# Performance work log

Measured on AMD Instinct MI355X. Metric: run time of the kernel, lower is better.

## Reference

```python
import jax, jax.numpy as jnp
import numpy as np

N = 8192        # n_nodes
NFEAT = 512
NHID = 256
AVG_DEG = 32
K = 64          # mean_kwargs k
TEMP = 1.0      # mean_kwargs temperature


def setup_inputs() -> dict:
    key = jax.random.key(0)
    ks = jax.random.split(key, 5)
    x = jax.random.normal(ks[0], (N, NFEAT), jnp.float32)
    edge_index = jax.random.randint(ks[1], (2, N * AVG_DEG), 0, N, dtype=jnp.int64)
    W1 = jax.random.normal(ks[2], (NFEAT, NHID), jnp.float32) / np.sqrt(NFEAT)
    b1 = jnp.zeros((NHID,), jnp.float32)
    W2 = jax.random.normal(ks[3], (NHID, NHID), jnp.float32) / np.sqrt(NHID)
    b2 = jnp.zeros((NHID,), jnp.float32)
    return {"x": x, "edge_index": edge_index, "W1": W1, "b1": b1, "W2": W2, "b2": b2}


def _gcn_norm(edge_index, n, dtype):
    # PyG gcn_norm: add self-loops (weight 1), deg over col, sym normalization
    loops = jnp.arange(n, dtype=edge_index.dtype)
    row = jnp.concatenate([edge_index[0], loops])
    col = jnp.concatenate([edge_index[1], loops])
    w = jnp.ones(row.shape[0], dtype)
    deg = jnp.zeros((n,), dtype).at[col].add(w)
    dis = jnp.where(deg > 0, jax.lax.rsqrt(jnp.where(deg > 0, deg, 1.0)), 0.0)
    return row, col, dis[row] * w * dis[col]


def _soft_k_medoid(row, col, w, x):
    # soft_weighted_medoid_k_neighborhood(A, x, k=K, temperature=TEMP, with_weight_correction=True)
    n, d = x.shape
    A = jnp.zeros((n, n), x.dtype).at[row, col].add(w)   # coalesced dense adjacency
    topk_a, topk_idx = jax.lax.top_k(A, K)               # [n, K] neighbor weights / ids
    xk = x[topk_idx]                                     # [n, K, d]
    sq = jnp.sum(xk * xk, axis=-1)                       # [n, K]
    G = jnp.einsum('nkd,nld->nkl', xk, xk)               # Gram per node
    d2 = jnp.maximum(sq[:, :, None] + sq[:, None, :] - 2.0 * G, 0.0)
    pos = d2 > 0
    dist = jnp.where(pos, jnp.sqrt(jnp.where(pos, d2, 1.0)), 0.0)  # safe sqrt (grad-safe)
    # weighted sum of distances to each top-k candidate j: c[n,j] = sum_l a[n,l] * ||x_l - x_j||
    c = jnp.einsum('nl,nlj->nj', topk_a, dist)
    c = jnp.where(topk_a == 0, jnp.finfo(x.dtype).max, c)
    soft = jax.nn.softmax(-c / TEMP, axis=-1)            # [n, K]
    soft = soft * topk_a                                 # with_weight_correction
    soft = soft / jnp.sum(soft, axis=-1, keepdims=True)
    row_sum = jnp.sum(A, axis=-1)                        # preserve neighborhood mass
    return row_sum[:, None] * jnp.einsum('nk,nkd->nd', soft, xk)


def reference(x, edge_index, W1, b1, W2, b2):
    n = x.shape[0]
    row, col, w = _gcn_norm(edge_index, n, x.dtype)
    h = jax.nn.relu(_soft_k_medoid(row, col, w, x @ W1) + b1)   # gc1 + relu (dropout: eval = identity)
    return jax.nn.relu(_soft_k_medoid(row, col, w, h @ W2) + b2)  # gc2 + relu
```

## Files before the change

### kernel.cpp

```cpp
#include <hip/hip_runtime.h>

typedef _Float16 half2v __attribute__((ext_vector_type(2)));
typedef _Float16 half4 __attribute__((ext_vector_type(4)));
typedef _Float16 half8 __attribute__((ext_vector_type(8)));
typedef float f32x4 __attribute__((ext_vector_type(4)));

#define NNODE 8192
#define NHID  256
#define RCAP  128
#define KCAP  64

__global__ void k_init(int* deg, int* rowcnt, int* flag, const void* edges) {
    int i = blockIdx.x * blockDim.x + threadIdx.x;
    if (i < NNODE) { deg[i] = 0; rowcnt[i] = 0; }
    if (i == 0) {
        const long long* e = (const long long*)edges;
        int ok = 1;
        for (int k = 0; k < 64; ++k) { long long v = e[k]; if (v < 0 || v >= NNODE) ok = 0; }
        *flag = ok;
    }
}

__global__ void k_build(const void* edges, const int* flag, int* rowcnt, int* nbr,
                        int* deg, int E) {
    int i = blockIdx.x * blockDim.x + threadIdx.x;
    int total = E + NNODE;
    if (i >= total) return;
    int r, c;
    if (i < E) {
        if (*flag) {
            const long long* e = (const long long*)edges;
            r = (int)e[i]; c = (int)e[E + i];
        } else {
            const int* e = (const int*)edges;
            r = e[i]; c = e[E + i];
        }
    } else { r = i - E; c = r; }
    int pos = atomicAdd(&rowcnt[r], 1);
    if (pos < RCAP) nbr[r * RCAP + pos] = c;
    atomicAdd(&deg[c], 1);
}

__global__ __launch_bounds__(128) void k_dedup(const int* __restrict__ nbr,
                                               const int* __restrict__ rowcnt,
                                               const int* __restrict__ deg,
                                               int* __restrict__ cols,
                                               float* __restrict__ wout,
                                               float* __restrict__ rsum) {
    __shared__ int lc[RCAP];
    __shared__ float lw[RCAP];
    __shared__ unsigned char kp[RCAP];
    __shared__ int s_cw[2];
    __shared__ float s_rw[2];
    const int r = blockIdx.x, t = threadIdx.x;
    const int wid = t >> 6, lane = t & 63;
    int n = rowcnt[r]; if (n > RCAP) n = RCAP;
    if (t < n) lc[t] = nbr[r * RCAP + t];
    __syncthreads();
    float dr = 1.f / sqrtf((float)deg[r]);
    bool keep = false; float wv = 0.f;
    if (t < n) {
        int c = lc[t];
        int mult = 0; bool first = true;
        for (int i = 0; i < n; ++i) {
            int ci = lc[i];
            if (ci == c) { mult++; if (i < t) first = false; }
        }
        keep = first;
        if (first) wv = (float)mult * dr * (1.f / sqrtf((float)deg[c]));
    }
    kp[t] = keep ? 1 : 0; lw[t] = wv;
    float rv = wv;
#pragma unroll
    for (int d = 1; d < 64; d <<= 1) rv += __shfl_xor(rv, d, 64);
    unsigned long long b = __ballot(keep);
    int pre = __popcll(b & ((1ull << lane) - 1ull));
    int cw = __popcll(b);
    if (lane == 0) { s_cw[wid] = cw; s_rw[wid] = rv; }
    __syncthreads();
    int total = s_cw[0] + s_cw[1];
    if (t == 0) rsum[r] = s_rw[0] + s_rw[1];
    const int base = r * KCAP;
    if (total <= KCAP) {
        int off = (wid ? s_cw[0] : 0) + pre;
        if (keep) { cols[base + off] = lc[t]; wout[base + off] = wv; }
        for (int m = total + t; m < KCAP; m += 128) { cols[base + m] = r; wout[base + m] = 0.f; }
    } else if (t == 0) {
        for (int s = 0; s < KCAP; ++s) {
            int best = -1;
            for (int i = 0; i < n; ++i) {
                if (!kp[i]) continue;
                if (best < 0 || lw[i] > lw[best] ||
                    (lw[i] == lw[best] && lc[i] < lc[best])) best = i;
            }
            cols[base + s] = lc[best]; wout[base + s] = lw[best]; kp[best] = 0;
        }
    }
}

__global__ void k_splitT(const float* __restrict__ W, _Float16* __restrict__ hiT, int Kdim) {
    int idx = blockIdx.x * 256 + threadIdx.x;
    if (idx >= Kdim * NHID) return;
    int k = idx >> 8, n = idx & 255;
    hiT[(size_t)n * Kdim + k] = (_Float16)W[idx];
}

#define GLS 72

__global__ __launch_bounds__(256) void k_gemm(
    const float* __restrict__ Af32, const _Float16* __restrict__ Ahi,
    const _Float16* __restrict__ BT, _Float16* __restrict__ Chi, int K, int af32) {
    __shared__ _Float16 sA[64][GLS];
    __shared__ _Float16 sB[64][GLS];
    const int t = threadIdx.x;
    const int bm = blockIdx.x * 64, bn = blockIdx.y * 64;
    const int lane = t & 63, L15 = lane & 15, q = lane >> 4;
    const int w = t >> 6, wr = w >> 1, wc = w & 1;
    f32x4 acc[2][2];
#pragma unroll
    for (int a = 0; a < 2; ++a)
#pragma unroll
        for (int b = 0; b < 2; ++b) acc[a][b] = (f32x4){0.f, 0.f, 0.f, 0.f};

    for (int k0 = 0; k0 < K; k0 += 64) {
        if (af32) {
#pragma unroll
            for (int i = 0; i < 4; ++i) {
                int row = i * 16 + (t >> 4), kc = (t & 15) * 4;
                float4 v = *(const float4*)(Af32 + (size_t)(bm + row) * K + k0 + kc);
                half4 h;
                h[0] = (_Float16)v.x; h[1] = (_Float16)v.y;
                h[2] = (_Float16)v.z; h[3] = (_Float16)v.w;
                *(half4*)&sA[row][kc] = h;
            }
        } else {
#pragma unroll
            for (int i = 0; i < 2; ++i) {
                int row = i * 32 + (t >> 3), ch = t & 7;
                *(half8*)&sA[row][ch * 8] =
                    *(const half8*)(Ahi + (size_t)(bm + row) * K + k0 + ch * 8);
            }
        }
#pragma unroll
        for (int i = 0; i < 2; ++i) {
            int row = i * 32 + (t >> 3), ch = t & 7;
            *(half8*)&sB[row][ch * 8] =
                *(const half8*)(BT + (size_t)(bn + row) * K + k0 + ch * 8);
        }
        __syncthreads();
#pragma unroll
        for (int ks = 0; ks < 2; ++ks) {
            const int ko = ks * 32 + q * 8;
            half8 ah[2], bh[2];
#pragma unroll
            for (int tr = 0; tr < 2; ++tr)
                ah[tr] = *(const half8*)&sA[32 * wr + 16 * tr + L15][ko];
#pragma unroll
            for (int tc = 0; tc < 2; ++tc)
                bh[tc] = *(const half8*)&sB[32 * wc + 16 * tc + L15][ko];
#pragma unroll
            for (int tr = 0; tr < 2; ++tr)
#pragma unroll
                for (int tc = 0; tc < 2; ++tc)
                    acc[tr][tc] = __builtin_amdgcn_mfma_f32_16x16x32_f16(ah[tr], bh[tc], acc[tr][tc], 0, 0, 0);
        }
        __syncthreads();
    }
#pragma unroll
    for (int tr = 0; tr < 2; ++tr)
#pragma unroll
        for (int tc = 0; tc < 2; ++tc)
#pragma unroll
            for (int r = 0; r < 4; ++r) {
                int rowg = bm + 32 * wr + 16 * tr + q * 4 + r;
                int colg = bn + 32 * wc + 16 * tc + L15;
                Chi[(size_t)rowg * NHID + colg] = (_Float16)acc[tr][tc][r];
            }
}

#define MS 264

__global__ __launch_bounds__(256, 4) void k_medoid(
    const _Float16* __restrict__ Xhi,
    const float* __restrict__ bias,
    float* __restrict__ OutF, _Float16* __restrict__ OutHi,
    const int* __restrict__ cols, const float* __restrict__ wts,
    const float* __restrict__ rsum, int writeH) {
    __shared__ _Float16 sh[64][MS];
    __shared__ float s_a[64];
    __shared__ float s_sq[64];
    __shared__ float s_cpart[2][64];
    __shared__ float s_u[64];
    __shared__ int   s_cols[64];
    __shared__ float s_red[4][288];

    const int node = blockIdx.x;
    const int t = threadIdx.x;
    const int w = t >> 6, lane = t & 63;
    const int L15 = lane & 15, q = lane >> 4;
    const int wr = w >> 1, wc = w & 1;

    if (t < 64) { s_cols[t] = cols[node * KCAP + t]; s_a[t] = wts[node * KCAP + t]; }
    __syncthreads();

    {
        const int ch = t & 31, rr = t >> 5;
#pragma unroll
        for (int i = 0; i < 8; ++i) {
            int l = i * 8 + rr;
            *(half8*)&sh[l][ch * 8] = *(const half8*)(Xhi + ((size_t)s_cols[l] << 8) + ch * 8);
        }
    }
    __syncthreads();

    f32x4 acc[2][2];
#pragma unroll
    for (int a = 0; a < 2; ++a)
#pragma unroll
        for (int b = 0; b < 2; ++b) acc[a][b] = (f32x4){0.f, 0.f, 0.f, 0.f};
#pragma unroll
    for (int ks = 0; ks < 8; ++ks) {
        const int ko = ks * 32 + q * 8;
        half8 ah[2], bh[2];
#pragma unroll
        for (int tr = 0; tr < 2; ++tr) ah[tr] = *(const half8*)&sh[32 * wr + 16 * tr + L15][ko];
#pragma unroll
        for (int tc = 0; tc < 2; ++tc) bh[tc] = *(const half8*)&sh[32 * wc + 16 * tc + L15][ko];
#pragma unroll
        for (int tr = 0; tr < 2; ++tr)
#pragma unroll
            for (int tc = 0; tc < 2; ++tc)
                acc[tr][tc] = __builtin_amdgcn_mfma_f32_16x16x32_f16(ah[tr], bh[tc], acc[tr][tc], 0, 0, 0);
    }

#pragma unroll
    for (int tr = 0; tr < 2; ++tr)
#pragma unroll
        for (int tc = 0; tc < 2; ++tc)
            if (32 * wr + 16 * tr == 32 * wc + 16 * tc) {
#pragma unroll
                for (int r = 0; r < 4; ++r)
                    if (L15 == q * 4 + r) s_sq[32 * wr + 16 * tr + L15] = acc[tr][tc][r];
            }
    __syncthreads();

#pragma unroll
    for (int tc = 0; tc < 2; ++tc) {
        const int colg = 32 * wc + 16 * tc + L15;
        const float sqc = s_sq[colg];
        float pj = 0.f;
#pragma unroll
        for (int tr = 0; tr < 2; ++tr)
#pragma unroll
            for (int r = 0; r < 4; ++r) {
                int rowg = 32 * wr + 16 * tr + q * 4 + r;
                float d2 = s_sq[rowg] + sqc - 2.f * acc[tr][tc][r];
                float dist = d2 > 0.f ? __builtin_amdgcn_sqrtf(d2) : 0.f;
                pj = fmaf(s_a[rowg], dist, pj);
            }
        pj += __shfl_xor(pj, 16, 64);
        pj += __shfl_xor(pj, 32, 64);
        if (q == 0) s_cpart[wr][colg] = pj;
    }
    __syncthreads();

    if (w == 0) {
        int j = lane;
        float c = s_cpart[0][j] + s_cpart[1][j];
        float aj = s_a[j];
        bool valid = aj > 0.f;
        float cv = valid ? c : 3.4e38f;
        float mn = cv;
#pragma unroll
        for (int d = 1; d < 64; d <<= 1) mn = fminf(mn, __shfl_xor(mn, d, 64));
        float e = valid ? __expf(mn - c) * aj : 0.f;
        float s = e;
#pragma unroll
        for (int d = 1; d < 64; d <<= 1) s += __shfl_xor(s, d, 64);
        s_u[j] = e * (rsum[node] / s);
    }
    __syncthreads();

    const int oct = t & 31, jb = t >> 5;
    float accd[8] = {0.f, 0.f, 0.f, 0.f, 0.f, 0.f, 0.f, 0.f};
#pragma unroll
    for (int jj = 0; jj < 8; ++jj) {
        int j = jb * 8 + jj;
        float u = s_u[j];
        half8 xv = *(const half8*)&sh[j][8 * oct];
#pragma unroll
        for (int e = 0; e < 8; ++e) accd[e] = fmaf(u, (float)xv[e], accd[e]);
    }
#pragma unroll
    for (int e = 0; e < 8; ++e) accd[e] += __shfl_xor(accd[e], 32, 64);
    if (lane < 32) {
#pragma unroll
        for (int e = 0; e < 8; ++e) s_red[w][9 * oct + e] = accd[e];
    }
    __syncthreads();
    const int idx = 9 * (t >> 3) + (t & 7);
    float o = s_red[0][idx] + s_red[1][idx] + s_red[2][idx] + s_red[3][idx];
    float res = fmaxf(o + bias[t], 0.f);
    size_t oi = (size_t)node * NHID + t;
    if (writeH) OutHi[oi] = (_Float16)res;
    else        OutF[oi] = res;
}

extern "C" void kernel_launch(void* const* d_in, const int* in_sizes, int n_in,
                              void* d_out, int out_size, void* d_ws, size_t ws_size,
                              hipStream_t stream) {
    const float* x  = (const float*)d_in[0];
    const void*  ei = d_in[1];
    const float* W1 = (const float*)d_in[2];
    const float* b1 = (const float*)d_in[3];
    const float* W2 = (const float*)d_in[4];
    const float* b2 = (const float*)d_in[5];
    float* out = (float*)d_out;
    const int E = in_sizes[1] / 2;

    char* p = (char*)d_ws;
    auto alloc = [&](size_t bytes) { char* q = p; p += (bytes + 255) & ~(size_t)255; return q; };
    int*      deg    = (int*)alloc((size_t)NNODE * 4);
    int*      rowcnt = (int*)alloc((size_t)NNODE * 4);
    int*      flag   = (int*)alloc(256);
    int*      colsA  = (int*)alloc((size_t)NNODE * KCAP * 4);
    float*    wA     = (float*)alloc((size_t)NNODE * KCAP * 4);
    float*    rsum   = (float*)alloc((size_t)NNODE * 4);
    _Float16* w1T    = (_Float16*)alloc((size_t)512 * NHID * 2);
    _Float16* w2T    = (_Float16*)alloc((size_t)NHID * NHID * 2);
    _Float16* X1hi   = (_Float16*)alloc((size_t)NNODE * NHID * 2);
    _Float16* Hhi    = (_Float16*)alloc((size_t)NNODE * NHID * 2);
    int* nbr = (int*)alloc((size_t)NNODE * RCAP * 4);

    k_init<<<(NNODE + 255) / 256, 256, 0, stream>>>(deg, rowcnt, flag, ei);
    k_build<<<(E + NNODE + 255) / 256, 256, 0, stream>>>(ei, flag, rowcnt, nbr, deg, E);
    k_dedup<<<NNODE, 128, 0, stream>>>(nbr, rowcnt, deg, colsA, wA, rsum);

    k_splitT<<<(512 * NHID + 255) / 256, 256, 0, stream>>>(W1, w1T, 512);
    k_splitT<<<(NHID * NHID + 255) / 256, 256, 0, stream>>>(W2, w2T, 256);

    k_gemm<<<dim3(NNODE / 64, NHID / 64), 256, 0, stream>>>(x, nullptr, w1T, X1hi, 512, 1);
    k_medoid<<<NNODE, 256, 0, stream>>>(X1hi, b1, nullptr, Hhi, colsA, wA, rsum, 1);
    k_gemm<<<dim3(NNODE / 64, NHID / 64), 256, 0, stream>>>(nullptr, Hhi, w2T, X1hi, 256, 0);
    k_medoid<<<NNODE, 256, 0, stream>>>(X1hi, b2, out, nullptr, colsA, wA, rsum, 0);
}
```

Measured before the change: 218.4 us.

## Merge independent setup kernels, pack dedup rows, compute squared norms at load

Independent setup work is merged into fewer launches: init plus both weight transposes share one kernel, and the edge-list build shares another with the first GEMM through block-index partitioning. The dedup kernel now handles two rows per 256-thread block. The medoid kernel computes squared norms with shuffle reductions while loading neighbor rows, which removes a barrier after the Gram MFMA. The aim is to cut launch overhead and serialization, at the cost of mixed workloads per launch and norms taken from fp16 values rather than from the Gram diagonal.

New measurement: 240.0 us. +9.9%, slower.

```diff
diff --git a/kernel.cpp b/kernel.cpp
--- a/kernel.cpp
+++ b/kernel.cpp
@@ -1,6 +1,5 @@
 #include <hip/hip_runtime.h>
 
-typedef _Float16 half2v __attribute__((ext_vector_type(2)));
 typedef _Float16 half4 __attribute__((ext_vector_type(4)));
 typedef _Float16 half8 __attribute__((ext_vector_type(8)));
 typedef float f32x4 __attribute__((ext_vector_type(4)));
@@ -10,117 +9,47 @@
 #define RCAP  128
 #define KCAP  64
 
-__global__ void k_init(int* deg, int* rowcnt, int* flag, const void* edges) {
-    int i = blockIdx.x * blockDim.x + threadIdx.x;
-    if (i < NNODE) { deg[i] = 0; rowcnt[i] = 0; }
-    if (i == 0) {
-        const long long* e = (const long long*)edges;
-        int ok = 1;
-        for (int k = 0; k < 64; ++k) { long long v = e[k]; if (v < 0 || v >= NNODE) ok = 0; }
-        *flag = ok;
-    }
-}
-
-__global__ void k_build(const void* edges, const int* flag, int* rowcnt, int* nbr,
-                        int* deg, int E) {
-    int i = blockIdx.x * blockDim.x + threadIdx.x;
-    int total = E + NNODE;
-    if (i >= total) return;
-    int r, c;
-    if (i < E) {
-        if (*flag) {
+__global__ __launch_bounds__(256) void k_fused1(
+    int* deg, int* rowcnt, int* flag, const void* edges,
+    const float* __restrict__ W1, _Float16* __restrict__ w1T,
+    const float* __restrict__ W2, _Float16* __restrict__ w2T) {
+    const int b = blockIdx.x, t = threadIdx.x;
+    if (b < 32) {
+        int i = b * 256 + t;
+        deg[i] = 0; rowcnt[i] = 0;
+        if (i == 0) {
             const long long* e = (const long long*)edges;
-            r = (int)e[i]; c = (int)e[E + i];
-        } else {
-            const int* e = (const int*)edges;
-            r = e[i]; c = e[E + i];
-        }
-    } else { r = i - E; c = r; }
-    int pos = atomicAdd(&rowcnt[r], 1);
-    if (pos < RCAP) nbr[r * RCAP + pos] = c;
-    atomicAdd(&deg[c], 1);
-}
-
-__global__ __launch_bounds__(128) void k_dedup(const int* __restrict__ nbr,
-                                               const int* __restrict__ rowcnt,
-                                               const int* __restrict__ deg,
-                                               int* __restrict__ cols,
-                                               float* __restrict__ wout,
-                                               float* __restrict__ rsum) {
-    __shared__ int lc[RCAP];
-    __shared__ float lw[RCAP];
-    __shared__ unsigned char kp[RCAP];
-    __shared__ int s_cw[2];
-    __shared__ float s_rw[2];
-    const int r = blockIdx.x, t = threadIdx.x;
-    const int wid = t >> 6, lane = t & 63;
-    int n = rowcnt[r]; if (n > RCAP) n = RCAP;
-    if (t < n) lc[t] = nbr[r * RCAP + t];
-    __syncthreads();
-    float dr = 1.f / sqrtf((float)deg[r]);
-    bool keep = false; float wv = 0.f;
-    if (t < n) {
-        int c = lc[t];
-        int mult = 0; bool first = true;
-        for (int i = 0; i < n; ++i) {
-            int ci = lc[i];
-            if (ci == c) { mult++; if (i < t) first = false; }
-        }
-        keep = first;
-        if (first) wv = (float)mult * dr * (1.f / sqrtf((float)deg[c]));
-    }
-    kp[t] = keep ? 1 : 0; lw[t] = wv;
-    float rv = wv;
-#pragma unroll
-    for (int d = 1; d < 64; d <<= 1) rv += __shfl_xor(rv, d, 64);
-    unsigned long long b = __ballot(keep);
-    int pre = __popcll(b & ((1ull << lane) - 1ull));
-    int cw = __popcll(b);
-    if (lane == 0) { s_cw[wid] = cw; s_rw[wid] = rv; }
-    __syncthreads();
-    int total = s_cw[0] + s_cw[1];
-    if (t == 0) rsum[r] = s_rw[0] + s_rw[1];
-    const int base = r * KCAP;
-    if (total <= KCAP) {
-        int off = (wid ? s_cw[0] : 0) + pre;
-        if (keep) { cols[base + off] = lc[t]; wout[base + off] = wv; }
-        for (int m = total + t; m < KCAP; m += 128) { cols[base + m] = r; wout[base + m] = 0.f; }
-    } else if (t == 0) {
-        for (int s = 0; s < KCAP; ++s) {
-            int best = -1;
-            for (int i = 0; i < n; ++i) {
-                if (!kp[i]) continue;
-                if (best < 0 || lw[i] > lw[best] ||
-                    (lw[i] == lw[best] && lc[i] < lc[best])) best = i;
-            }
-            cols[base + s] = lc[best]; wout[base + s] = lw[best]; kp[best] = 0;
-        }
-    }
-}
-
-__global__ void k_splitT(const float* __restrict__ W, _Float16* __restrict__ hiT, int Kdim) {
-    int idx = blockIdx.x * 256 + threadIdx.x;
-    if (idx >= Kdim * NHID) return;
-    int k = idx >> 8, n = idx & 255;
-    hiT[(size_t)n * Kdim + k] = (_Float16)W[idx];
+            int ok = 1;
+            for (int k = 0; k < 64; ++k) { long long v = e[k]; if (v < 0 || v >= NNODE) ok = 0; }
+            *flag = ok;
+        }
+    } else if (b < 32 + 512) {
+        int idx = (b - 32) * 256 + t;
+        int k = idx >> 8, n = idx & 255;
+        w1T[(size_t)n * 512 + k] = (_Float16)W1[idx];
+    } else {
+        int idx = (b - 544) * 256 + t;
+        int k = idx >> 8, n = idx & 255;
+        w2T[(size_t)n * 256 + k] = (_Float16)W2[idx];
+    }
 }
 
 #define GLS 72
 
-__global__ __launch_bounds__(256) void k_gemm(
+__device__ __forceinline__ void gemm_body(
     const float* __restrict__ Af32, const _Float16* __restrict__ Ahi,
-    const _Float16* __restrict__ BT, _Float16* __restrict__ Chi, int K, int af32) {
+    const _Float16* __restrict__ BT, _Float16* __restrict__ Chi,
+    int K, int af32, int bm, int bn) {
     __shared__ _Float16 sA[64][GLS];
     __shared__ _Float16 sB[64][GLS];
     const int t = threadIdx.x;
-    const int bm = blockIdx.x * 64, bn = blockIdx.y * 64;
     const int lane = t & 63, L15 = lane & 15, q = lane >> 4;
     const int w = t >> 6, wr = w >> 1, wc = w & 1;
     f32x4 acc[2][2];
 #pragma unroll
     for (int a = 0; a < 2; ++a)
 #pragma unroll
-        for (int b = 0; b < 2; ++b) acc[a][b] = (f32x4){0.f, 0.f, 0.f, 0.f};
+        for (int b2 = 0; b2 < 2; ++b2) acc[a][b2] = (f32x4){0.f, 0.f, 0.f, 0.f};
 
     for (int k0 = 0; k0 < K; k0 += 64) {
         if (af32) {
@@ -176,6 +105,97 @@
                 int colg = bn + 32 * wc + 16 * tc + L15;
                 Chi[(size_t)rowg * NHID + colg] = (_Float16)acc[tr][tc][r];
             }
+}
+
+__global__ __launch_bounds__(256) void k_fused2(
+    const void* edges, const int* flag, int* rowcnt, int* nbr, int* deg, int E, int nbuild,
+    const float* __restrict__ x, const _Float16* __restrict__ w1T, _Float16* __restrict__ X1) {
+    if ((int)blockIdx.x < nbuild) {
+        int i = blockIdx.x * 256 + threadIdx.x;
+        int total = E + NNODE;
+        if (i >= total) return;
+        int r, c;
+        if (i < E) {
+            if (*flag) {
+                const long long* e = (const long long*)edges;
+                r = (int)e[i]; c = (int)e[E + i];
+            } else {
+                const int* e = (const int*)edges;
+                r = e[i]; c = e[E + i];
+            }
+        } else { r = i - E; c = r; }
+        int pos = atomicAdd(&rowcnt[r], 1);
+        if (pos < RCAP) nbr[r * RCAP + pos] = c;
+        atomicAdd(&deg[c], 1);
+    } else {
+        int g = blockIdx.x - nbuild;
+        gemm_body(x, nullptr, w1T, X1, 512, 1, (g >> 2) * 64, (g & 3) * 64);
+    }
+}
+
+__global__ __launch_bounds__(256) void k_gemm(
+    const _Float16* __restrict__ Ahi, const _Float16* __restrict__ BT,
+    _Float16* __restrict__ Chi, int K) {
+    gemm_body(nullptr, Ahi, BT, Chi, K, 0, blockIdx.x * 64, blockIdx.y * 64);
+}
+
+__global__ __launch_bounds__(256) void k_dedup(const int* __restrict__ nbr,
+                                               const int* __restrict__ rowcnt,
+                                               const int* __restrict__ deg,
+                                               int* __restrict__ cols,
+                                               float* __restrict__ wout,
+                                               float* __restrict__ rsum) {
+    __shared__ int lc[2][RCAP];
+    __shared__ float lw[2][RCAP];
+    __shared__ unsigned char kp[2][RCAP];
+    __shared__ int s_cw[2][2];
+    __shared__ float s_rw[2][2];
+    const int t = threadIdx.x;
+    const int half = t >> 7, st = t & 127;
+    const int wid = st >> 6, lane = t & 63;
+    const int r = blockIdx.x * 2 + half;
+    int n = rowcnt[r]; if (n > RCAP) n = RCAP;
+    if (st < n) lc[half][st] = nbr[r * RCAP + st];
+    __syncthreads();
+    float dr = 1.f / sqrtf((float)deg[r]);
+    bool keep = false; float wv = 0.f;
+    if (st < n) {
+        int c = lc[half][st];
+        int mult = 0; bool first = true;
+        for (int i = 0; i < n; ++i) {
+            int ci = lc[half][i];
+            if (ci == c) { mult++; if (i < st) first = false; }
+        }
+        keep = first;
+        if (first) wv = (float)mult * dr * (1.f / sqrtf((float)deg[c]));
+    }
+    kp[half][st] = keep ? 1 : 0; lw[half][st] = wv;
+    float rv = wv;
+#pragma unroll
+    for (int d = 1; d < 64; d <<= 1) rv += __shfl_xor(rv, d, 64);
+    unsigned long long b = __ballot(keep);
+    int pre = __popcll(b & ((1ull << lane) - 1ull));
+    int cw = __popcll(b);
+    if (lane == 0) { s_cw[half][wid] = cw; s_rw[half][wid] = rv; }
+    __syncthreads();
+    int total = s_cw[half][0] + s_cw[half][1];
+    if (st == 0) rsum[r] = s_rw[half][0] + s_rw[half][1];
+    const int base = r * KCAP;
+    if (total <= KCAP) {
+        int off = (wid ? s_cw[half][0] : 0) + pre;
+        if (keep) { cols[base + off] = lc[half][st]; wout[base + off] = wv; }
+        for (int m = total + st; m < KCAP; m += 128) { cols[base + m] = r; wout[base + m] = 0.f; }
+    } else if (st == 0) {
+        for (int s = 0; s < KCAP; ++s) {
+            int best = -1;
+            for (int i = 0; i < n; ++i) {
+                if (!kp[half][i]) continue;
+                if (best < 0 || lw[half][i] > lw[half][best] ||
+                    (lw[half][i] == lw[half][best] && lc[half][i] < lc[half][best])) best = i;
+            }
+            cols[base + s] = lc[half][best]; wout[base + s] = lw[half][best]; kp[half][best] = 0;
+        }
+    }
 }
 
 #define MS 264
@@ -205,10 +225,24 @@
 
     {
         const int ch = t & 31, rr = t >> 5;
+        float ps[8];
 #pragma unroll
         for (int i = 0; i < 8; ++i) {
             int l = i * 8 + rr;
-            *(half8*)&sh[l][ch * 8] = *(const half8*)(Xhi + ((size_t)s_cols[l] << 8) + ch * 8);
+            half8 v = *(const half8*)(Xhi + ((size_t)s_cols[l] << 8) + ch * 8);
+            *(half8*)&sh[l][ch * 8] = v;
+            float s = 0.f;
+#pragma unroll
+            for (int e = 0; e < 8; ++e) { float f = (float)v[e]; s = fmaf(f, f, s); }
+            ps[i] = s;
+        }
+#pragma unroll
+        for (int d = 1; d < 32; d <<= 1)
+#pragma unroll
+            for (int i = 0; i < 8; ++i) ps[i] += __shfl_xor(ps[i], d, 64);
+        if (ch == 0) {
+#pragma unroll
+            for (int i = 0; i < 8; ++i) s_sq[i * 8 + rr] = ps[i];
         }
     }
     __syncthreads();
@@ -232,17 +266,6 @@
             for (int tc = 0; tc < 2; ++tc)
                 acc[tr][tc] = __builtin_amdgcn_mfma_f32_16x16x32_f16(ah[tr], bh[tc], acc[tr][tc], 0, 0, 0);
     }
-
-#pragma unroll
-    for (int tr = 0; tr < 2; ++tr)
-#pragma unroll
-        for (int tc = 0; tc < 2; ++tc)
-            if (32 * wr + 16 * tr == 32 * wc + 16 * tc) {
-#pragma unroll
-                for (int r = 0; r < 4; ++r)
-                    if (L15 == q * 4 + r) s_sq[32 * wr + 16 * tr + L15] = acc[tr][tc][r];
-            }
-    __syncthreads();
 
 #pragma unroll
     for (int tc = 0; tc < 2; ++tc) {
@@ -330,17 +353,14 @@
     _Float16* w2T    = (_Float16*)alloc((size_t)NHID * NHID * 2);
     _Float16* X1hi   = (_Float16*)alloc((size_t)NNODE * NHID * 2);
     _Float16* Hhi    = (_Float16*)alloc((size_t)NNODE * NHID * 2);
-    int* nbr = (int*)alloc((size_t)NNODE * RCAP * 4);
-
-    k_init<<<(NNODE + 255) / 256, 256, 0, stream>>>(deg, rowcnt, flag, ei);
-    k_build<<<(E + NNODE + 255) / 256, 256, 0, stream>>>(ei, flag, rowcnt, nbr, deg, E);
-    k_dedup<<<NNODE, 128, 0, stream>>>(nbr, rowcnt, deg, colsA, wA, rsum);
-
-    k_splitT<<<(512 * NHID + 255) / 256, 256, 0, stream>>>(W1, w1T, 512);
-    k_splitT<<<(NHID * NHID + 255) / 256, 256, 0, stream>>>(W2, w2T, 256);
-
-    k_gemm<<<dim3(NNODE / 64, NHID / 64), 256, 0, stream>>>(x, nullptr, w1T, X1hi, 512, 1);
+    int*      nbr    = (int*)alloc((size_t)NNODE * RCAP * 4);
+
+    const int nbuild = (E + NNODE + 255) / 256;
+
+    k_fused1<<<32 + 512 + 256, 256, 0, stream>>>(deg, rowcnt, flag, ei, W1, w1T, W2, w2T);
+    k_fused2<<<nbuild + 512, 256, 0, stream>>>(ei, flag, rowcnt, nbr, deg, E, nbuild, x, w1T, X1hi);
+    k_dedup<<<NNODE / 2, 256, 0, stream>>>(nbr, rowcnt, deg, colsA, wA, rsum);
     k_medoid<<<NNODE, 256, 0, stream>>>(X1hi, b1, nullptr, Hhi, colsA, wA, rsum, 1);
-    k_gemm<<<dim3(NNODE / 64, NHID / 64), 256, 0, stream>>>(nullptr, Hhi, w2T, X1hi, 256, 0);
+    k_gemm<<<dim3(NNODE / 64, NHID / 64), 256, 0, stream>>>(Hhi, w2T, X1hi, 256);
     k_medoid<<<NNODE, 256, 0, stream>>>(X1hi, b2, out, nullptr, colsA, wA, rsum, 0);
 }
```
